# Kernel optimization log

Hardware: AMD Instinct MI355X
Metric: run time of the kernel (lower is better)

Reference implementation:

```python
import jax, jax.numpy as jnp
import numpy as np

FORMULA_OH_SIZES = [20, 20, 20, 20, 20]
SPECT_BIN_N = 512


def layer_norm(x, g, b, eps=1e-5):
    m = jnp.mean(x, axis=-1, keepdims=True)
    v = jnp.var(x, axis=-1, keepdims=True)
    return (x - m) * jax.lax.rsqrt(v + eps) * g + b


def gru_cell(x, h, W_ih, W_hh, b_ih, b_hh):
    # torch.nn.GRUCell math
    gi = x @ W_ih.T + b_ih
    gh = h @ W_hh.T + b_hh
    i_r, i_z, i_n = jnp.split(gi, 3, axis=-1)
    h_r, h_z, h_n = jnp.split(gh, 3, axis=-1)
    r = jax.nn.sigmoid(i_r + h_r)
    z = jax.nn.sigmoid(i_z + h_z)
    n = jnp.tanh(i_n + r * h_n)
    return (1.0 - z) * n + z * h


def structured_one_hot(x, sizes, accum=True):
    # x: [N, len(sizes)] integer element counts -> concatenated (accumulated) one-hots
    outs = []
    for i, s in enumerate(sizes):
        v = jnp.clip(x[:, i].astype(jnp.int32), 0, s - 1)
        if accum:
            oh = (jnp.arange(s)[None, :] <= v[:, None]).astype(jnp.float32)  # thermometer
        else:
            oh = jax.nn.one_hot(v, s, dtype=jnp.float32)
        outs.append(oh)
    return jnp.concatenate(outs, axis=-1)


def setup_inputs():
    key = jax.random.key(0)
    ks = jax.random.split(key, 16)
    B, A, GF, HW, S, M = 16, 32, 128, 4, 4096, 8
    G = GF * HW                       # 512 = g_feat_in * highway_steps_n
    FE = sum(FORMULA_OH_SIZES)        # 100
    D = 512                           # internal_d
    vert_feat_in = jax.random.normal(ks[0], (B, A, GF, HW), jnp.float32)
    vert_mask_in = jnp.ones((B, A), jnp.float32)
    elem_id = jax.random.randint(ks[1], (B, A), 0, 5)
    vert_element_oh = jax.nn.one_hot(elem_id, 5, dtype=jnp.float32)
    adj_oh = jnp.zeros((B, A, A, 4), jnp.float32)  # unused by forward
    atom_subsets = jax.random.bernoulli(ks[2], 0.5, (B, S, A)).astype(jnp.float32)
    masses = jax.random.uniform(ks[3], (B, S, M), jnp.float32, 0.0, SPECT_BIN_N - 1.0)
    intens = jax.random.uniform(ks[4], (B, S, M), jnp.float32)
    atom_subsets_peaks = jnp.stack([masses, intens], axis=-1)

    def lin(k, o, i):
        return (jax.random.normal(k, (o, i), jnp.float32) / np.sqrt(i)).astype(jnp.float32)

    return dict(
        vert_feat_in=vert_feat_in, vert_mask_in=vert_mask_in,
        vert_element_oh=vert_element_oh, adj_oh=adj_oh,
        atom_subsets=atom_subsets, atom_subsets_peaks=atom_subsets_peaks,
        ln_sub_g=jnp.ones((G,), jnp.float32), ln_sub_b=jnp.zeros((G,), jnp.float32),
        W_ih=lin(ks[5], 3 * G, FE), W_hh=lin(ks[6], 3 * G, G),
        b_ih=jnp.zeros((3 * G,), jnp.float32), b_hh=jnp.zeros((3 * G,), jnp.float32),
        W1=lin(ks[7], D, G), b1=jnp.zeros((D,), jnp.float32),
        W2a=lin(ks[8], D, D), b2a=jnp.zeros((D,), jnp.float32),
        W2b=lin(ks[9], D, D), b2b=jnp.zeros((D,), jnp.float32),
        ln_pre_g=jnp.ones((D,), jnp.float32), ln_pre_b=jnp.zeros((D,), jnp.float32),
        Ws=lin(ks[10], 1, D), bs=jnp.zeros((1,), jnp.float32),
    )


def reference(vert_feat_in, vert_mask_in, vert_element_oh, adj_oh, atom_subsets,
              atom_subsets_peaks, ln_sub_g, ln_sub_b, W_ih, W_hh, b_ih, b_hh,
              W1, b1, W2a, b2a, W2b, b2b, ln_pre_g, ln_pre_b, Ws, bs):
    B, A, GF, HW = vert_feat_in.shape
    S = atom_subsets.shape[1]
    vf = vert_feat_in.reshape(B, A, GF * HW)                       # [B,A,G]
    masked_vf = vf * vert_mask_in[:, :, None]
    subs_m = atom_subsets * vert_mask_in[:, None, :]               # [B,S,A]
    swvs = jnp.einsum('bag,bsa->bsg', masked_vf, subs_m)           # [B,S,G]
    # per-subset element counts -> structured one-hot formula encoding
    counts = jnp.einsum('bae,bsa->bse', vert_element_oh, atom_subsets).astype(jnp.int32)
    pf_flat = structured_one_hot(counts.reshape(B * S, -1), FORMULA_OH_SIZES, accum=True)
    subset_size = jnp.sum(subs_m, axis=2) + 1e-4                   # [B,S]
    mean = swvs / subset_size[:, :, None]
    normed = layer_norm(mean, ln_sub_g, ln_sub_b)                  # [B,S,G]
    h = gru_cell(pf_flat, normed.reshape(B * S, -1), W_ih, W_hh, b_ih, b_hh)
    h = h.reshape(normed.shape)
    x = jax.nn.relu(h @ W1.T + b1)
    x = jax.nn.relu(x @ W2a.T + b2a)
    x = jax.nn.relu(x @ W2b.T + b2b)   # (extra F.relu in original is idempotent)
    x = layer_norm(x, ln_pre_g, ln_pre_b)
    scores = (x @ Ws.T + bs)[..., 0]                               # [B,S]
    probs = jax.nn.softmax(scores, axis=-1)
    # mass histogram: scatter intensity*prob into rounded-mass bins
    masses = atom_subsets_peaks[..., 0]                            # [B,S,M]
    intens = atom_subsets_peaks[..., 1]
    bins = jnp.clip(jnp.round(masses).astype(jnp.int32), 0, SPECT_BIN_N - 1)
    contrib = intens * probs[:, :, None]                           # [B,S,M]
    spect = jnp.zeros((B, SPECT_BIN_N), x.dtype).at[
        jnp.arange(B)[:, None], bins.reshape(B, -1)].add(contrib.reshape(B, -1))
    return (spect, probs)
```

## Files before the change

kernel.cpp:

```cpp
#include <hip/hip_runtime.h>
#include <math.h>

#define B_ 16
#define A_ 32
#define G_ 512
#define S_ 4096
#define M_ 8
#define BS_ 65536
#define KC_ 640
#define NG_ 1536

typedef _Float16 half8 __attribute__((ext_vector_type(8)));
typedef _Float16 half4v __attribute__((ext_vector_type(4)));
typedef _Float16 half2v __attribute__((ext_vector_type(2)));
typedef float floatx4 __attribute__((ext_vector_type(4)));

typedef const __attribute__((address_space(1))) void* gas_t;
typedef __attribute__((address_space(3))) void* las_t;

__device__ __forceinline__ float wave_sum_f(float v){
#pragma unroll
  for (int o = 32; o > 0; o >>= 1) v += __shfl_xor(v, o);
  return v;
}
__device__ __forceinline__ float wave_max_f(float v){
#pragma unroll
  for (int o = 32; o > 0; o >>= 1) v = fmaxf(v, __shfl_xor(v, o));
  return v;
}
__device__ __forceinline__ float sigmoidf_(float x){ return 1.f/(1.f+__expf(-x)); }
__device__ __forceinline__ float tanhf_(float x){ return 1.f - 2.f/(__expf(2.f*x)+1.f); }

__global__ __launch_bounds__(256) void k_cvt(const float* __restrict__ s,
                                             _Float16* __restrict__ d, int n){
  int i = (blockIdx.x*256 + threadIdx.x)*4;
  if (i >= n) return;
  float4 v = *(const float4*)(s+i);
  half4v o; o[0]=(_Float16)v.x; o[1]=(_Float16)v.y; o[2]=(_Float16)v.z; o[3]=(_Float16)v.w;
  *(half4v*)(d+i) = o;
}

__global__ __launch_bounds__(64) void k_buildw(const float* __restrict__ Whh,
                                               const float* __restrict__ Wih,
                                               _Float16* __restrict__ Wcat){
  int j = blockIdx.x;
  for (int p = threadIdx.x; p < KC_; p += 64){
    float v = 0.f;
    if (p < 512) v = Whh[(size_t)j*512 + p];
    else if (p < 612) v = Wih[(size_t)j*100 + (p - 512)];
    Wcat[(size_t)j*KC_ + p] = (_Float16)v;
  }
}

__global__ __launch_bounds__(256) void k_prep_mfma(
    const float* __restrict__ vf, const float* __restrict__ mask,
    const float* __restrict__ eoh, const float* __restrict__ subs,
    const float* __restrict__ ln_g, const float* __restrict__ ln_b,
    _Float16* __restrict__ Abuf){
  __shared__ _Float16 s_mvfT[G_*A_];
  __shared__ _Float16 s_sm[128*A_];
  __shared__ float s_m[A_];
  __shared__ float s_e[A_*5];
  __shared__ float s_ssum[128];
  __shared__ float s_red1[4][16];
  __shared__ float s_red2[4][16];
  int tid = threadIdx.x;
  int bx = blockIdx.x, b = blockIdx.y;
  int lane = tid & 63, w = tid >> 6;
  int q = lane >> 4, l15 = lane & 15;
  size_t row0 = (size_t)b*S_ + (size_t)bx*128;
  if (tid < A_)   s_m[tid] = mask[b*A_ + tid];
  if (tid < A_*5) s_e[tid] = eoh[b*A_*5 + tid];
  __syncthreads();
  {
    int p = tid & 15, gseg = tid >> 4;
    float mk0 = s_m[2*p], mk1 = s_m[2*p+1];
    const float* v0 = vf + ((size_t)b*A_ + 2*p)*G_ + gseg*32;
    const float* v1 = v0 + G_;
#pragma unroll
    for (int i = 0; i < 32; ++i){
      int g = gseg*32 + i;
      half2v h; h[0] = (_Float16)(v0[i]*mk0); h[1] = (_Float16)(v1[i]*mk1);
      *(half2v*)(s_mvfT + g*A_ + 2*p) = h;
    }
  }
  {
    int s = tid >> 1, hh = tid & 1;
    const float* sp = subs + (row0 + s)*A_ + hh*16;
#pragma unroll
    for (int i = 0; i < 16; i += 2){
      half2v h; h[0] = (_Float16)sp[i]; h[1] = (_Float16)sp[i+1];
      *(half2v*)(s_sm + s*A_ + hh*16 + i) = h;
    }
  }
  __syncthreads();
  if (tid < 128){
    int s = tid;
    float ssum = 0.f, c0=0.f, c1=0.f, c2=0.f, c3=0.f, c4=0.f;
#pragma unroll
    for (int a = 0; a < A_; ++a){
      float v = (float)s_sm[s*A_ + a];
      ssum += v * s_m[a];
      c0 += v * s_e[a*5+0]; c1 += v * s_e[a*5+1]; c2 += v * s_e[a*5+2];
      c3 += v * s_e[a*5+3]; c4 += v * s_e[a*5+4];
    }
    int cc[5];
    cc[0] = min(max((int)(c0+0.5f),0),19); cc[1] = min(max((int)(c1+0.5f),0),19);
    cc[2] = min(max((int)(c2+0.5f),0),19); cc[3] = min(max((int)(c3+0.5f),0),19);
    cc[4] = min(max((int)(c4+0.5f),0),19);
    s_ssum[s] = ssum;
    _Float16* dst = Abuf + (row0 + s)*KC_ + 512;
#pragma unroll
    for (int t = 0; t < 16; ++t){
      half8 hv;
#pragma unroll
      for (int u = 0; u < 8; ++u){
        int k = t*8 + u;
        float v = 0.f;
        if (k < 100){ int f = k/20, l = k - f*20; v = (l <= cc[f]) ? 1.f : 0.f; }
        hv[u] = (_Float16)v;
      }
      *(half8*)(dst + t*8) = hv;
    }
  }
  half8 bf[8]; float lng[8], lnb[8];
#pragma unroll
  for (int t = 0; t < 8; ++t){
    int g = w*128 + t*16 + l15;
    bf[t] = *(const half8*)(s_mvfT + g*A_ + q*8);
    lng[t] = ln_g[g]; lnb[t] = ln_b[g];
  }
  __syncthreads();
  for (int gi = 0; gi < 8; ++gi){
    half8 af = *(const half8*)(s_sm + (gi*16 + l15)*A_ + q*8);
    floatx4 c[8];
#pragma unroll
    for (int t = 0; t < 8; ++t){
      floatx4 z = {0.f, 0.f, 0.f, 0.f};
      c[t] = __builtin_amdgcn_mfma_f32_16x16x32_f16(af, bf[t], z, 0, 0, 0);
    }
    float p1[4] = {0.f,0.f,0.f,0.f}, p2[4] = {0.f,0.f,0.f,0.f};
#pragma unroll
    for (int t = 0; t < 8; ++t)
#pragma unroll
      for (int r = 0; r < 4; ++r){ float v = c[t][r]; p1[r] += v; p2[r] += v*v; }
#pragma unroll
    for (int off = 1; off < 16; off <<= 1)
#pragma unroll
      for (int r = 0; r < 4; ++r){
        p1[r] += __shfl_xor(p1[r], off);
        p2[r] += __shfl_xor(p2[r], off);
      }
    if (l15 == 0){
#pragma unroll
      for (int r = 0; r < 4; ++r){ s_red1[w][q*4+r] = p1[r]; s_red2[w][q*4+r] = p2[r]; }
    }
    __syncthreads();
#pragma unroll
    for (int r = 0; r < 4; ++r){
      int sl = gi*16 + q*4 + r;
      int rr = q*4 + r;
      float t1 = s_red1[0][rr] + s_red1[1][rr] + s_red1[2][rr] + s_red1[3][rr];
      float t2 = s_red2[0][rr] + s_red2[1][rr] + s_red2[2][rr] + s_red2[3][rr];
      float inv = 1.f/(s_ssum[sl] + 1e-4f);
      float mu = t1*inv*(1.f/512.f);
      float var = t2*inv*inv*(1.f/512.f) - mu*mu;
      float rs = rsqrtf(var + 1e-5f);
      _Float16* orow = Abuf + (row0 + sl)*KC_;
#pragma unroll
      for (int t = 0; t < 8; ++t){
        float o = (c[t][r]*inv - mu)*rs*lng[t] + lnb[t];
        orow[w*128 + t*16 + l15] = (_Float16)o;
      }
    }
    __syncthreads();
  }
}

__global__ __launch_bounds__(512) void k_gru_fused(
    const _Float16* __restrict__ Abuf, const _Float16* __restrict__ Wcat,
    const float* __restrict__ bih, const float* __restrict__ bhh,
    _Float16* __restrict__ H){
  __shared__ _Float16 smA[128*32];
  __shared__ _Float16 smB[192*32];
  int tid = threadIdx.x;
  int lane = tid & 63, wvid = tid >> 6;
  int wm = wvid & 1, wn = wvid >> 1;
  int q = lane >> 4, l15 = lane & 15;
  int mt = blockIdx.x*64 + (blockIdx.y >> 3);
  int dt = blockIdx.y & 7;
  int m0 = mt*128, n0 = dt*64;
  floatx4 acc[3][4] = {};
  floatx4 accNI[4] = {};
  int offA[4], offB[3];
#pragma unroll
  for (int i = 0; i < 4; ++i){
    int r = wm*64 + i*16 + l15;
    offA[i] = (r*4 + (q ^ ((r>>2)&3)))*8;
  }
#pragma unroll
  for (int g = 0; g < 3; ++g){
    int rb = g*64 + wn*16 + l15;
    offB[g] = (rb*4 + (q ^ ((rb>>2)&3)))*8;
  }
  const _Float16* gA;
  {
    int u = wvid*64 + lane;
    int r = u >> 2, c = (u & 3) ^ ((r >> 2) & 3);
    gA = Abuf + (size_t)(m0 + r)*KC_ + c*8;
  }
  const _Float16* gB0;
  {
    int u = wvid*64 + lane;
    int rb = u >> 2, c = (u & 3) ^ ((rb >> 2) & 3);
    int grow = (rb >> 6)*512 + n0 + (rb & 63);
    gB0 = Wcat + (size_t)grow*KC_ + c*8;
  }
  const _Float16* gB1 = nullptr;
  if (wvid < 4){
    int u = (8 + wvid)*64 + lane;
    int rb = u >> 2, c = (u & 3) ^ ((rb >> 2) & 3);
    int grow = (rb >> 6)*512 + n0 + (rb & 63);
    gB1 = Wcat + (size_t)grow*KC_ + c*8;
  }
  for (int kc = 0; kc < 512; kc += 32){
    __builtin_amdgcn_global_load_lds((gas_t)(gA + kc), (las_t)(smA + wvid*512), 16, 0, 0);
    __builtin_amdgcn_global_load_lds((gas_t)(gB0 + kc), (las_t)(smB + wvid*512), 16, 0, 0);
    if (wvid < 4)
      __builtin_amdgcn_global_load_lds((gas_t)(gB1 + kc), (las_t)(smB + (8+wvid)*512), 16, 0, 0);
    __syncthreads();
    half8 af[4], bfv[3];
#pragma unroll
    for (int i = 0; i < 4; ++i) af[i] = *(const half8*)(smA + offA[i]);
#pragma unroll
    for (int g = 0; g < 3; ++g) bfv[g] = *(const half8*)(smB + offB[g]);
#pragma unroll
    for (int g = 0; g < 3; ++g)
#pragma unroll
      for (int i = 0; i < 4; ++i)
        acc[g][i] = __builtin_amdgcn_mfma_f32_16x16x32_f16(af[i], bfv[g], acc[g][i], 0, 0, 0);
    __syncthreads();
  }
  for (int kc = 512; kc < KC_; kc += 32){
    __builtin_amdgcn_global_load_lds((gas_t)(gA + kc), (las_t)(smA + wvid*512), 16, 0, 0);
    __builtin_amdgcn_global_load_lds((gas_t)(gB0 + kc), (las_t)(smB + wvid*512), 16, 0, 0);
    if (wvid < 4)
      __builtin_amdgcn_global_load_lds((gas_t)(gB1 + kc), (las_t)(smB + (8+wvid)*512), 16, 0, 0);
    __syncthreads();
    half8 af[4], bfv[3];
#pragma unroll
    for (int i = 0; i < 4; ++i) af[i] = *(const half8*)(smA + offA[i]);
#pragma unroll
    for (int g = 0; g < 3; ++g) bfv[g] = *(const half8*)(smB + offB[g]);
#pragma unroll
    for (int i = 0; i < 4; ++i){
      acc[0][i] = __builtin_amdgcn_mfma_f32_16x16x32_f16(af[i], bfv[0], acc[0][i], 0, 0, 0);
      acc[1][i] = __builtin_amdgcn_mfma_f32_16x16x32_f16(af[i], bfv[1], acc[1][i], 0, 0, 0);
      accNI[i]  = __builtin_amdgcn_mfma_f32_16x16x32_f16(af[i], bfv[2], accNI[i], 0, 0, 0);
    }
    __syncthreads();
  }
  int d = n0 + wn*16 + l15;
  float br  = bih[d] + bhh[d];
  float bz  = bih[512+d] + bhh[512+d];
  float bnh = bhh[1024+d];
  float bni = bih[1024+d];
#pragma unroll
  for (int i = 0; i < 4; ++i){
#pragma unroll
    for (int r = 0; r < 4; ++r){
      int m = m0 + wm*64 + i*16 + q*4 + r;
      float gr  = acc[0][i][r] + br;
      float gz  = acc[1][i][r] + bz;
      float hn  = acc[2][i][r] + bnh;
      float in_ = accNI[i][r] + bni;
      float rrv = sigmoidf_(gr);
      float zz  = sigmoidf_(gz);
      float nn  = tanhf_(in_ + rrv*hn);
      float hp  = (float)Abuf[(size_t)m*KC_ + d];
      H[(size_t)m*G_ + d] = (_Float16)((1.f-zz)*nn + zz*hp);
    }
  }
}

__global__ __launch_bounds__(256) void k_gemm(
    const _Float16* __restrict__ A, const _Float16* __restrict__ W,
    const float* __restrict__ bias, _Float16* __restrict__ Out){
  __shared__ _Float16 smA[128*32];
  __shared__ _Float16 smB[128*32];
  int tid = threadIdx.x;
  int lane = tid & 63, wvid = tid >> 6;
  int wm = wvid & 1, wn = wvid >> 1;
  int q = lane >> 4, l15 = lane & 15;
  int mt = blockIdx.x*64 + (blockIdx.y >> 2);
  int nt = blockIdx.y & 3;
  int m0 = mt*128, n0 = nt*128;
  floatx4 acc[4][4] = {};
  int offA[4], offB[4];
#pragma unroll
  for (int i = 0; i < 4; ++i){
    int r = wm*64 + i*16 + l15;
    offA[i] = (r*4 + (q ^ ((r>>2)&3)))*8;
    int rb = wn*64 + i*16 + l15;
    offB[i] = (rb*4 + (q ^ ((rb>>2)&3)))*8;
  }
  int uA[2];
  const _Float16 *gA[2], *gB[2];
#pragma unroll
  for (int t = 0; t < 2; ++t){
    int seg = wvid*2 + t;
    int u = seg*64 + lane;
    int r = u >> 2, c = (u & 3) ^ ((r >> 2) & 3);
    uA[t] = seg;
    gA[t] = A + (size_t)(m0 + r)*G_ + c*8;
    gB[t] = W + (size_t)(n0 + r)*G_ + c*8;
  }
  for (int kc = 0; kc < G_; kc += 32){
#pragma unroll
    for (int t = 0; t < 2; ++t){
      __builtin_amdgcn_global_load_lds((gas_t)(gA[t] + kc), (las_t)(smA + uA[t]*512), 16, 0, 0);
      __builtin_amdgcn_global_load_lds((gas_t)(gB[t] + kc), (las_t)(smB + uA[t]*512), 16, 0, 0);
    }
    __syncthreads();
    half8 af[4], bfv[4];
#pragma unroll
    for (int i = 0; i < 4; ++i) af[i] = *(const half8*)(smA + offA[i]);
#pragma unroll
    for (int j = 0; j < 4; ++j) bfv[j] = *(const half8*)(smB + offB[j]);
#pragma unroll
    for (int i = 0; i < 4; ++i)
#pragma unroll
      for (int j = 0; j < 4; ++j)
        acc[i][j] = __builtin_amdgcn_mfma_f32_16x16x32_f16(af[i], bfv[j], acc[i][j], 0, 0, 0);
    __syncthreads();
  }
#pragma unroll
  for (int j = 0; j < 4; ++j){
    int n = n0 + wn*64 + j*16 + l15;
    float bv = bias[n];
#pragma unroll
    for (int i = 0; i < 4; ++i){
#pragma unroll
      for (int r = 0; r < 4; ++r){
        int m = m0 + wm*64 + i*16 + q*4 + r;
        Out[(size_t)m*G_ + n] = (_Float16)fmaxf(acc[i][j][r] + bv, 0.f);
      }
    }
  }
}

__global__ __launch_bounds__(256) void k_ln_score(
    const _Float16* __restrict__ X, const float* __restrict__ g,
    const float* __restrict__ bta, const float* __restrict__ Ws,
    const float* __restrict__ bs, float* __restrict__ scores){
  int tid = threadIdx.x, lane = tid & 63, wv = tid >> 6;
  size_t row0 = (size_t)blockIdx.x*32 + wv*8;
  int e0 = lane*8;
  float wv_[8], gv[8], bv[8];
  *(float4*)(wv_ ) = *(const float4*)(Ws + e0);
  *(float4*)(wv_+4) = *(const float4*)(Ws + e0 + 4);
  *(float4*)(gv  ) = *(const float4*)(g + e0);
  *(float4*)(gv+4) = *(const float4*)(g + e0 + 4);
  *(float4*)(bv  ) = *(const float4*)(bta + e0);
  *(float4*)(bv+4) = *(const float4*)(bta + e0 + 4);
  float bsv = bs[0];
  for (int rr = 0; rr < 8; ++rr){
    size_t row = row0 + rr;
    half8 hx = *(const half8*)(X + row*G_ + e0);
    float xv[8];
#pragma unroll
    for (int t = 0; t < 8; ++t) xv[t] = (float)hx[t];
    float s1 = 0.f, s2 = 0.f;
#pragma unroll
    for (int t = 0; t < 8; ++t){ s1 += xv[t]; s2 += xv[t]*xv[t]; }
    s1 = wave_sum_f(s1); s2 = wave_sum_f(s2);
    float mu = s1*(1.f/512.f);
    float var = s2*(1.f/512.f) - mu*mu;
    float rs = rsqrtf(var + 1e-5f);
    float sc = 0.f;
#pragma unroll
    for (int t = 0; t < 8; ++t) sc += ((xv[t]-mu)*rs*gv[t] + bv[t])*wv_[t];
    sc = wave_sum_f(sc);
    if (lane == 0) scores[row] = sc + bsv;
  }
}

__global__ __launch_bounds__(256) void k_softmax(
    const float* __restrict__ scores, float* __restrict__ probs){
  __shared__ float red[4];
  int b = blockIdx.x, tid = threadIdx.x, lane = tid & 63, wv = tid >> 6;
  const float* sp = scores + (size_t)b*S_;
  float mx = -1e30f;
  for (int i = tid; i < S_; i += 256) mx = fmaxf(mx, sp[i]);
  mx = wave_max_f(mx);
  if (lane == 0) red[wv] = mx;
  __syncthreads();
  mx = fmaxf(fmaxf(red[0], red[1]), fmaxf(red[2], red[3]));
  __syncthreads();
  float sum = 0.f;
  for (int i = tid; i < S_; i += 256) sum += __expf(sp[i]-mx);
  sum = wave_sum_f(sum);
  if (lane == 0) red[wv] = sum;
  __syncthreads();
  sum = red[0]+red[1]+red[2]+red[3];
  float inv = 1.f/sum;
  for (int i = tid; i < S_; i += 256)
    probs[(size_t)b*S_ + i] = __expf(sp[i]-mx)*inv;
}

__global__ __launch_bounds__(256) void k_spect(
    const float* __restrict__ peaks, const float* __restrict__ probs,
    float* __restrict__ spect){
  __shared__ float bins[512];
  int b = blockIdx.x, tid = threadIdx.x;
  bins[tid] = 0.f; bins[tid+256] = 0.f;
  __syncthreads();
  for (int i = tid; i < S_*M_; i += 256){
    int s = i >> 3, m = i & 7;
    const float* pk = peaks + (((size_t)b*S_ + s)*M_ + m)*2;
    float mass = pk[0], inten = pk[1];
    float p = probs[(size_t)b*S_ + s];
    int bin = (int)rintf(mass);
    bin = min(max(bin, 0), 511);
    atomicAdd(&bins[bin], inten*p);
  }
  __syncthreads();
  spect[(size_t)b*512 + tid]       = bins[tid];
  spect[(size_t)b*512 + tid + 256] = bins[tid+256];
}

extern "C" void kernel_launch(void* const* d_in, const int* in_sizes, int n_in,
                              void* d_out, int out_size, void* d_ws, size_t ws_size,
                              hipStream_t stream) {
  const float* vf       = (const float*)d_in[0];
  const float* mask     = (const float*)d_in[1];
  const float* eoh      = (const float*)d_in[2];
  const float* subs     = (const float*)d_in[4];
  const float* peaks    = (const float*)d_in[5];
  const float* ln_sub_g = (const float*)d_in[6];
  const float* ln_sub_b = (const float*)d_in[7];
  const float* W_ih     = (const float*)d_in[8];
  const float* W_hh     = (const float*)d_in[9];
  const float* b_ih     = (const float*)d_in[10];
  const float* b_hh     = (const float*)d_in[11];
  const float* W1       = (const float*)d_in[12];
  const float* b1       = (const float*)d_in[13];
  const float* W2a      = (const float*)d_in[14];
  const float* b2a      = (const float*)d_in[15];
  const float* W2b      = (const float*)d_in[16];
  const float* b2b      = (const float*)d_in[17];
  const float* ln_pre_g = (const float*)d_in[18];
  const float* ln_pre_b = (const float*)d_in[19];
  const float* Ws       = (const float*)d_in[20];
  const float* bs       = (const float*)d_in[21];
  float* out = (float*)d_out;
  float* probs_out = out + (size_t)B_*512;

  char* w = (char*)d_ws;
  float* scores = (float*)w;     w += (size_t)BS_*4;
  _Float16* Wcat = (_Float16*)w; w += (size_t)NG_*KC_*2;
  _Float16* W1h  = (_Float16*)w; w += (size_t)G_*G_*2;
  _Float16* W2ah = (_Float16*)w; w += (size_t)G_*G_*2;
  _Float16* W2bh = (_Float16*)w; w += (size_t)G_*G_*2;
  _Float16* Abuf = (_Float16*)w; w += (size_t)BS_*KC_*2;
  _Float16* bufh0 = (_Float16*)w;
  _Float16* bufh1 = Abuf;

  k_cvt<<<(G_*G_/4+255)/256, 256, 0, stream>>>(W1,  W1h,  G_*G_);
  k_cvt<<<(G_*G_/4+255)/256, 256, 0, stream>>>(W2a, W2ah, G_*G_);
  k_cvt<<<(G_*G_/4+255)/256, 256, 0, stream>>>(W2b, W2bh, G_*G_);
  k_buildw<<<NG_, 64, 0, stream>>>(W_hh, W_ih, Wcat);
  k_prep_mfma<<<dim3(S_/128, B_), 256, 0, stream>>>(vf, mask, eoh, subs,
                                                    ln_sub_g, ln_sub_b, Abuf);
  k_gru_fused<<<dim3(8, 512), 512, 0, stream>>>(Abuf, Wcat, b_ih, b_hh, bufh0);
  k_gemm<<<dim3(8, 256), 256, 0, stream>>>(bufh0, W1h,  b1,  bufh1);
  k_gemm<<<dim3(8, 256), 256, 0, stream>>>(bufh1, W2ah, b2a, bufh0);
  k_gemm<<<dim3(8, 256), 256, 0, stream>>>(bufh0, W2bh, b2b, bufh1);
  k_ln_score<<<BS_/32, 256, 0, stream>>>(bufh1, ln_pre_g, ln_pre_b, Ws, bs, scores);
  k_softmax<<<B_, 256, 0, stream>>>(scores, probs_out);
  k_spect<<<B_, 256, 0, stream>>>(peaks, probs_out, out);
}
```

Measured before the change: 522.8 us.

## Fuse final FF layer with layernorm-score partials, widen GEMM K-tile, vectorize prep loads

The third feed-forward GEMM now computes per-row partial sums (sum, sum of squares, gamma·Ws dot) in its epilogue, and a small kernel turns them into layernorm-projected scores. This avoids writing and re-reading the full fp16 activation. GEMMs move to a 64-wide K tile with an 8-way XOR swizzle, which halves barrier count at the cost of more LDS. The three weight conversions merge into one launch, the prep kernel uses float4 loads, and it double-buffers its reduction scratch to drop a barrier. The algebraic layernorm-dot rewrite uses a one-pass variance and may lose some precision.

New measurement: 535.5 us. 2.4% more time.

```diff
diff --git a/kernel.cpp b/kernel.cpp
--- a/kernel.cpp
+++ b/kernel.cpp
@@ -31,13 +31,16 @@
 __device__ __forceinline__ float sigmoidf_(float x){ return 1.f/(1.f+__expf(-x)); }
 __device__ __forceinline__ float tanhf_(float x){ return 1.f - 2.f/(__expf(2.f*x)+1.f); }
 
-__global__ __launch_bounds__(256) void k_cvt(const float* __restrict__ s,
-                                             _Float16* __restrict__ d, int n){
+__global__ __launch_bounds__(256) void k_cvt3(const float* __restrict__ s0,
+                                              const float* __restrict__ s1,
+                                              const float* __restrict__ s2,
+                                              _Float16* __restrict__ d){
+  const float* s = (blockIdx.y == 0) ? s0 : (blockIdx.y == 1) ? s1 : s2;
   int i = (blockIdx.x*256 + threadIdx.x)*4;
-  if (i >= n) return;
+  if (i >= G_*G_) return;
   float4 v = *(const float4*)(s+i);
   half4v o; o[0]=(_Float16)v.x; o[1]=(_Float16)v.y; o[2]=(_Float16)v.z; o[3]=(_Float16)v.w;
-  *(half4v*)(d+i) = o;
+  *(half4v*)(d + (size_t)blockIdx.y*G_*G_ + i) = o;
 }
 
 __global__ __launch_bounds__(64) void k_buildw(const float* __restrict__ Whh,
@@ -62,8 +65,8 @@
   __shared__ float s_m[A_];
   __shared__ float s_e[A_*5];
   __shared__ float s_ssum[128];
-  __shared__ float s_red1[4][16];
-  __shared__ float s_red2[4][16];
+  __shared__ float s_red1[2][4][16];
+  __shared__ float s_red2[2][4][16];
   int tid = threadIdx.x;
   int bx = blockIdx.x, b = blockIdx.y;
   int lane = tid & 63, w = tid >> 6;
@@ -78,19 +81,27 @@
     const float* v0 = vf + ((size_t)b*A_ + 2*p)*G_ + gseg*32;
     const float* v1 = v0 + G_;
 #pragma unroll
-    for (int i = 0; i < 32; ++i){
-      int g = gseg*32 + i;
-      half2v h; h[0] = (_Float16)(v0[i]*mk0); h[1] = (_Float16)(v1[i]*mk1);
-      *(half2v*)(s_mvfT + g*A_ + 2*p) = h;
+    for (int i = 0; i < 32; i += 4){
+      float4 a = *(const float4*)(v0 + i);
+      float4 c = *(const float4*)(v1 + i);
+      float av[4] = {a.x, a.y, a.z, a.w};
+      float cv[4] = {c.x, c.y, c.z, c.w};
+#pragma unroll
+      for (int j = 0; j < 4; ++j){
+        half2v h; h[0] = (_Float16)(av[j]*mk0); h[1] = (_Float16)(cv[j]*mk1);
+        *(half2v*)(s_mvfT + (gseg*32 + i + j)*A_ + 2*p) = h;
+      }
     }
   }
   {
     int s = tid >> 1, hh = tid & 1;
     const float* sp = subs + (row0 + s)*A_ + hh*16;
-#pragma unroll
-    for (int i = 0; i < 16; i += 2){
-      half2v h; h[0] = (_Float16)sp[i]; h[1] = (_Float16)sp[i+1];
-      *(half2v*)(s_sm + s*A_ + hh*16 + i) = h;
+    _Float16* dst = s_sm + s*A_ + hh*16;
+#pragma unroll
+    for (int i = 0; i < 16; i += 4){
+      float4 v = *(const float4*)(sp + i);
+      half4v h; h[0]=(_Float16)v.x; h[1]=(_Float16)v.y; h[2]=(_Float16)v.z; h[3]=(_Float16)v.w;
+      *(half4v*)(dst + i) = h;
     }
   }
   __syncthreads();
@@ -151,17 +162,18 @@
         p1[r] += __shfl_xor(p1[r], off);
         p2[r] += __shfl_xor(p2[r], off);
       }
+    int gb = gi & 1;
     if (l15 == 0){
 #pragma unroll
-      for (int r = 0; r < 4; ++r){ s_red1[w][q*4+r] = p1[r]; s_red2[w][q*4+r] = p2[r]; }
+      for (int r = 0; r < 4; ++r){ s_red1[gb][w][q*4+r] = p1[r]; s_red2[gb][w][q*4+r] = p2[r]; }
     }
     __syncthreads();
 #pragma unroll
     for (int r = 0; r < 4; ++r){
       int sl = gi*16 + q*4 + r;
       int rr = q*4 + r;
-      float t1 = s_red1[0][rr] + s_red1[1][rr] + s_red1[2][rr] + s_red1[3][rr];
-      float t2 = s_red2[0][rr] + s_red2[1][rr] + s_red2[2][rr] + s_red2[3][rr];
+      float t1 = s_red1[gb][0][rr] + s_red1[gb][1][rr] + s_red1[gb][2][rr] + s_red1[gb][3][rr];
+      float t2 = s_red2[gb][0][rr] + s_red2[gb][1][rr] + s_red2[gb][2][rr] + s_red2[gb][3][rr];
       float inv = 1.f/(s_ssum[sl] + 1e-4f);
       float mu = t1*inv*(1.f/512.f);
       float var = t2*inv*inv*(1.f/512.f) - mu*mu;
@@ -173,7 +185,6 @@
         orow[w*128 + t*16 + l15] = (_Float16)o;
       }
     }
-    __syncthreads();
   }
 }
 
@@ -283,11 +294,11 @@
   }
 }
 
-__global__ __launch_bounds__(256) void k_gemm(
+__global__ __launch_bounds__(256) void k_gemm64(
     const _Float16* __restrict__ A, const _Float16* __restrict__ W,
     const float* __restrict__ bias, _Float16* __restrict__ Out){
-  __shared__ _Float16 smA[128*32];
-  __shared__ _Float16 smB[128*32];
+  __shared__ _Float16 smA[128*64];
+  __shared__ _Float16 smB[128*64];
   int tid = threadIdx.x;
   int lane = tid & 63, wvid = tid >> 6;
   int wm = wvid & 1, wn = wvid >> 1;
@@ -296,42 +307,46 @@
   int nt = blockIdx.y & 3;
   int m0 = mt*128, n0 = nt*128;
   floatx4 acc[4][4] = {};
-  int offA[4], offB[4];
-#pragma unroll
-  for (int i = 0; i < 4; ++i){
-    int r = wm*64 + i*16 + l15;
-    offA[i] = (r*4 + (q ^ ((r>>2)&3)))*8;
-    int rb = wn*64 + i*16 + l15;
-    offB[i] = (rb*4 + (q ^ ((rb>>2)&3)))*8;
-  }
-  int uA[2];
-  const _Float16 *gA[2], *gB[2];
-#pragma unroll
-  for (int t = 0; t < 2; ++t){
-    int seg = wvid*2 + t;
+  int offA[2][4], offB[2][4];
+#pragma unroll
+  for (int s = 0; s < 2; ++s)
+#pragma unroll
+    for (int i = 0; i < 4; ++i){
+      int r = wm*64 + i*16 + l15;
+      offA[s][i] = r*64 + (((s*4+q) ^ (r&7))*8);
+      int rb = wn*64 + i*16 + l15;
+      offB[s][i] = rb*64 + (((s*4+q) ^ (rb&7))*8);
+    }
+  const _Float16 *gA[4], *gB[4]; int so[4];
+#pragma unroll
+  for (int t = 0; t < 4; ++t){
+    int seg = wvid*4 + t;
     int u = seg*64 + lane;
-    int r = u >> 2, c = (u & 3) ^ ((r >> 2) & 3);
-    uA[t] = seg;
+    int r = u >> 3, c = (u & 7) ^ (r & 7);
+    so[t] = seg*512;
     gA[t] = A + (size_t)(m0 + r)*G_ + c*8;
     gB[t] = W + (size_t)(n0 + r)*G_ + c*8;
   }
-  for (int kc = 0; kc < G_; kc += 32){
-#pragma unroll
-    for (int t = 0; t < 2; ++t){
-      __builtin_amdgcn_global_load_lds((gas_t)(gA[t] + kc), (las_t)(smA + uA[t]*512), 16, 0, 0);
-      __builtin_amdgcn_global_load_lds((gas_t)(gB[t] + kc), (las_t)(smB + uA[t]*512), 16, 0, 0);
-    }
-    __syncthreads();
-    half8 af[4], bfv[4];
-#pragma unroll
-    for (int i = 0; i < 4; ++i) af[i] = *(const half8*)(smA + offA[i]);
-#pragma unroll
-    for (int j = 0; j < 4; ++j) bfv[j] = *(const half8*)(smB + offB[j]);
-#pragma unroll
-    for (int i = 0; i < 4; ++i)
-#pragma unroll
-      for (int j = 0; j < 4; ++j)
-        acc[i][j] = __builtin_amdgcn_mfma_f32_16x16x32_f16(af[i], bfv[j], acc[i][j], 0, 0, 0);
+  for (int kc = 0; kc < G_; kc += 64){
+#pragma unroll
+    for (int t = 0; t < 4; ++t){
+      __builtin_amdgcn_global_load_lds((gas_t)(gA[t] + kc), (las_t)(smA + so[t]), 16, 0, 0);
+      __builtin_amdgcn_global_load_lds((gas_t)(gB[t] + kc), (las_t)(smB + so[t]), 16, 0, 0);
+    }
+    __syncthreads();
+#pragma unroll
+    for (int s = 0; s < 2; ++s){
+      half8 af[4], bfv[4];
+#pragma unroll
+      for (int i = 0; i < 4; ++i) af[i] = *(const half8*)(smA + offA[s][i]);
+#pragma unroll
+      for (int j = 0; j < 4; ++j) bfv[j] = *(const half8*)(smB + offB[s][j]);
+#pragma unroll
+      for (int i = 0; i < 4; ++i)
+#pragma unroll
+        for (int j = 0; j < 4; ++j)
+          acc[i][j] = __builtin_amdgcn_mfma_f32_16x16x32_f16(af[i], bfv[j], acc[i][j], 0, 0, 0);
+    }
     __syncthreads();
   }
 #pragma unroll
@@ -349,40 +364,129 @@
   }
 }
 
-__global__ __launch_bounds__(256) void k_ln_score(
-    const _Float16* __restrict__ X, const float* __restrict__ g,
+__global__ __launch_bounds__(256) void k_ff3_fin(
+    const _Float16* __restrict__ A, const _Float16* __restrict__ W,
+    const float* __restrict__ bias, const float* __restrict__ ln_pre_g,
+    const float* __restrict__ Ws, float* __restrict__ Pbuf){
+  __shared__ _Float16 smA[128*64];
+  __shared__ _Float16 smB[128*64];
+  __shared__ float sP[2][64][2][3];
+  int tid = threadIdx.x;
+  int lane = tid & 63, wvid = tid >> 6;
+  int wm = wvid & 1, wn = wvid >> 1;
+  int q = lane >> 4, l15 = lane & 15;
+  int mt = blockIdx.x*64 + (blockIdx.y >> 2);
+  int nt = blockIdx.y & 3;
+  int m0 = mt*128, n0 = nt*128;
+  floatx4 acc[4][4] = {};
+  int offA[2][4], offB[2][4];
+#pragma unroll
+  for (int s = 0; s < 2; ++s)
+#pragma unroll
+    for (int i = 0; i < 4; ++i){
+      int r = wm*64 + i*16 + l15;
+      offA[s][i] = r*64 + (((s*4+q) ^ (r&7))*8);
+      int rb = wn*64 + i*16 + l15;
+      offB[s][i] = rb*64 + (((s*4+q) ^ (rb&7))*8);
+    }
+  const _Float16 *gA[4], *gB[4]; int so[4];
+#pragma unroll
+  for (int t = 0; t < 4; ++t){
+    int seg = wvid*4 + t;
+    int u = seg*64 + lane;
+    int r = u >> 3, c = (u & 7) ^ (r & 7);
+    so[t] = seg*512;
+    gA[t] = A + (size_t)(m0 + r)*G_ + c*8;
+    gB[t] = W + (size_t)(n0 + r)*G_ + c*8;
+  }
+  for (int kc = 0; kc < G_; kc += 64){
+#pragma unroll
+    for (int t = 0; t < 4; ++t){
+      __builtin_amdgcn_global_load_lds((gas_t)(gA[t] + kc), (las_t)(smA + so[t]), 16, 0, 0);
+      __builtin_amdgcn_global_load_lds((gas_t)(gB[t] + kc), (las_t)(smB + so[t]), 16, 0, 0);
+    }
+    __syncthreads();
+#pragma unroll
+    for (int s = 0; s < 2; ++s){
+      half8 af[4], bfv[4];
+#pragma unroll
+      for (int i = 0; i < 4; ++i) af[i] = *(const half8*)(smA + offA[s][i]);
+#pragma unroll
+      for (int j = 0; j < 4; ++j) bfv[j] = *(const half8*)(smB + offB[s][j]);
+#pragma unroll
+      for (int i = 0; i < 4; ++i)
+#pragma unroll
+        for (int j = 0; j < 4; ++j)
+          acc[i][j] = __builtin_amdgcn_mfma_f32_16x16x32_f16(af[i], bfv[j], acc[i][j], 0, 0, 0);
+    }
+    __syncthreads();
+  }
+  float gws[4], bv4[4];
+#pragma unroll
+  for (int j = 0; j < 4; ++j){
+    int n = n0 + wn*64 + j*16 + l15;
+    gws[j] = ln_pre_g[n]*Ws[n];
+    bv4[j] = bias[n];
+  }
+#pragma unroll
+  for (int i = 0; i < 4; ++i){
+#pragma unroll
+    for (int r = 0; r < 4; ++r){
+      float p1 = 0.f, p2 = 0.f, p3 = 0.f;
+#pragma unroll
+      for (int j = 0; j < 4; ++j){
+        float x = fmaxf(acc[i][j][r] + bv4[j], 0.f);
+        p1 += x; p2 += x*x; p3 += gws[j]*x;
+      }
+#pragma unroll
+      for (int off = 1; off < 16; off <<= 1){
+        p1 += __shfl_xor(p1, off);
+        p2 += __shfl_xor(p2, off);
+        p3 += __shfl_xor(p3, off);
+      }
+      if (l15 == 0){
+        int rl = i*16 + q*4 + r;
+        sP[wm][rl][wn][0] = p1; sP[wm][rl][wn][1] = p2; sP[wm][rl][wn][2] = p3;
+      }
+    }
+  }
+  __syncthreads();
+  if (tid < 128){
+    int wmi = tid >> 6, rl = tid & 63;
+    int m = m0 + wmi*64 + rl;
+    float* dst = Pbuf + ((size_t)m*4 + nt)*3;
+    dst[0] = sP[wmi][rl][0][0] + sP[wmi][rl][1][0];
+    dst[1] = sP[wmi][rl][0][1] + sP[wmi][rl][1][1];
+    dst[2] = sP[wmi][rl][0][2] + sP[wmi][rl][1][2];
+  }
+}
+
+__global__ __launch_bounds__(256) void k_score_fin(
+    const float* __restrict__ Pbuf, const float* __restrict__ g,
     const float* __restrict__ bta, const float* __restrict__ Ws,
     const float* __restrict__ bs, float* __restrict__ scores){
+  __shared__ float red[8];
   int tid = threadIdx.x, lane = tid & 63, wv = tid >> 6;
-  size_t row0 = (size_t)blockIdx.x*32 + wv*8;
-  int e0 = lane*8;
-  float wv_[8], gv[8], bv[8];
-  *(float4*)(wv_ ) = *(const float4*)(Ws + e0);
-  *(float4*)(wv_+4) = *(const float4*)(Ws + e0 + 4);
-  *(float4*)(gv  ) = *(const float4*)(g + e0);
-  *(float4*)(gv+4) = *(const float4*)(g + e0 + 4);
-  *(float4*)(bv  ) = *(const float4*)(bta + e0);
-  *(float4*)(bv+4) = *(const float4*)(bta + e0 + 4);
-  float bsv = bs[0];
-  for (int rr = 0; rr < 8; ++rr){
-    size_t row = row0 + rr;
-    half8 hx = *(const half8*)(X + row*G_ + e0);
-    float xv[8];
-#pragma unroll
-    for (int t = 0; t < 8; ++t) xv[t] = (float)hx[t];
-    float s1 = 0.f, s2 = 0.f;
-#pragma unroll
-    for (int t = 0; t < 8; ++t){ s1 += xv[t]; s2 += xv[t]*xv[t]; }
-    s1 = wave_sum_f(s1); s2 = wave_sum_f(s2);
-    float mu = s1*(1.f/512.f);
-    float var = s2*(1.f/512.f) - mu*mu;
-    float rs = rsqrtf(var + 1e-5f);
-    float sc = 0.f;
-#pragma unroll
-    for (int t = 0; t < 8; ++t) sc += ((xv[t]-mu)*rs*gv[t] + bv[t])*wv_[t];
-    sc = wave_sum_f(sc);
-    if (lane == 0) scores[row] = sc + bsv;
-  }
+  int i0 = tid*2;
+  float c1p = g[i0]*Ws[i0] + g[i0+1]*Ws[i0+1];
+  float c2p = bta[i0]*Ws[i0] + bta[i0+1]*Ws[i0+1];
+  c1p = wave_sum_f(c1p); c2p = wave_sum_f(c2p);
+  if (lane == 0){ red[wv] = c1p; red[4+wv] = c2p; }
+  __syncthreads();
+  float c1 = red[0]+red[1]+red[2]+red[3];
+  float c2 = red[4]+red[5]+red[6]+red[7] + bs[0];
+  size_t row = (size_t)blockIdx.x*256 + tid;
+  const float* p = Pbuf + row*12;
+  float4 a  = *(const float4*)p;
+  float4 b4 = *(const float4*)(p+4);
+  float4 c4 = *(const float4*)(p+8);
+  float P1 = a.x + a.w + b4.z + c4.y;
+  float P2 = a.y + b4.x + b4.w + c4.z;
+  float P3 = a.z + b4.y + c4.x + c4.w;
+  float mu = P1*(1.f/512.f);
+  float var = P2*(1.f/512.f) - mu*mu;
+  float rs = rsqrtf(var + 1e-5f);
+  scores[row] = rs*(P3 - mu*c1) + c2;
 }
 
 __global__ __launch_bounds__(256) void k_softmax(
@@ -458,6 +562,7 @@
 
   char* w = (char*)d_ws;
   float* scores = (float*)w;     w += (size_t)BS_*4;
+  float* Pbuf   = (float*)w;     w += (size_t)BS_*12*4;
   _Float16* Wcat = (_Float16*)w; w += (size_t)NG_*KC_*2;
   _Float16* W1h  = (_Float16*)w; w += (size_t)G_*G_*2;
   _Float16* W2ah = (_Float16*)w; w += (size_t)G_*G_*2;
@@ -466,17 +571,16 @@
   _Float16* bufh0 = (_Float16*)w;
   _Float16* bufh1 = Abuf;
 
-  k_cvt<<<(G_*G_/4+255)/256, 256, 0, stream>>>(W1,  W1h,  G_*G_);
-  k_cvt<<<(G_*G_/4+255)/256, 256, 0, stream>>>(W2a, W2ah, G_*G_);
-  k_cvt<<<(G_*G_/4+255)/256, 256, 0, stream>>>(W2b, W2bh, G_*G_);
+  k_cvt3<<<dim3((G_*G_/4+255)/256, 3), 256, 0, stream>>>(W1, W2a, W2b, W1h);
   k_buildw<<<NG_, 64, 0, stream>>>(W_hh, W_ih, Wcat);
   k_prep_mfma<<<dim3(S_/128, B_), 256, 0, stream>>>(vf, mask, eoh, subs,
                                                     ln_sub_g, ln_sub_b, Abuf);
   k_gru_fused<<<dim3(8, 512), 512, 0, stream>>>(Abuf, Wcat, b_ih, b_hh, bufh0);
-  k_gemm<<<dim3(8, 256), 256, 0, stream>>>(bufh0, W1h,  b1,  bufh1);
-  k_gemm<<<dim3(8, 256), 256, 0, stream>>>(bufh1, W2ah, b2a, bufh0);
-  k_gemm<<<dim3(8, 256), 256, 0, stream>>>(bufh0, W2bh, b2b, bufh1);
-  k_ln_score<<<BS_/32, 256, 0, stream>>>(bufh1, ln_pre_g, ln_pre_b, Ws, bs, scores);
+  k_gemm64<<<dim3(8, 256), 256, 0, stream>>>(bufh0, W1h,  b1,  bufh1);
+  k_gemm64<<<dim3(8, 256), 256, 0, stream>>>(bufh1, W2ah, b2a, bufh0);
+  k_ff3_fin<<<dim3(8, 256), 256, 0, stream>>>(bufh0, W2bh, b2b,
+                                              ln_pre_g, Ws, Pbuf);
+  k_score_fin<<<BS_/256, 256, 0, stream>>>(Pbuf, ln_pre_g, ln_pre_b, Ws, bs, scores);
   k_softmax<<<B_, 256, 0, stream>>>(scores, probs_out);
   k_spect<<<B_, 256, 0, stream>>>(peaks, probs_out, out);
 }
```
